# Kernel tuning notes

Measured on AMD Instinct MI355X. Metric: run time of the kernel, lower is better.

The kernel has to match this reference:

```python
import jax, jax.numpy as jnp
import numpy as np

EPS = 1e-5
NEG_SLOPE = 0.2
B, C, P, K, E, H = 16, 16, 2048, 16, 64, 2


def cross_set_gather(f, idx):
    # f: (B, C, P), idx: (B, P, K) -> (B, C, P, K)
    return jax.vmap(lambda fb, ib: fb[:, ib])(f, idx)


def bn(x, g, b, m, v, axes):
    # x normalized along channel dim; g,b,m,v shaped to broadcast via `axes` reshape
    return (x - m.reshape(axes)) * (g.reshape(axes) / jnp.sqrt(v.reshape(axes) + EPS)) + b.reshape(axes)


def setup_inputs() -> dict:
    key = jax.random.key(0)
    ks = jax.random.split(key, 16)
    features = jax.random.normal(ks[0], (B, C, P), dtype=jnp.float32)
    neighbor_indices = jax.random.randint(ks[1], (B, P, K), 0, P)
    mask = jax.random.randint(ks[2], (B, 1, P), 0, 2).astype(bool)
    s = 0.1
    return {
        "features": features,
        "neighbor_indices": neighbor_indices,
        "mask": mask,
        "node_w": jax.random.normal(ks[3], (H, E, C)) * s,
        "node_g": jnp.ones((H, E)),
        "node_b": jnp.zeros((H, E)),
        "node_m": jax.random.normal(ks[4], (H, E)) * s,
        "node_v": jax.random.uniform(ks[5], (H, E)) + 0.5,
        "edge_w": jax.random.normal(ks[6], (H, E, C)) * s,
        "edge_bias": jax.random.normal(ks[7], (H, E)) * s,
        "edge_g": jnp.ones((H, E)),
        "edge_b2": jnp.zeros((H, E)),
        "edge_m": jax.random.normal(ks[8], (H, E)) * s,
        "edge_v": jax.random.uniform(ks[9], (H, E)) + 0.5,
        "self_w": jax.random.normal(ks[10], (H, E)) * s,
        "self_b": jax.random.normal(ks[11], (H,)) * s,
        "nb_w": jax.random.normal(ks[12], (H, E)) * s,
        "nb_b": jax.random.normal(ks[13], (H,)) * s,
    }


def _forward(features, neighbor_indices, mask, node_w, node_g, node_b, node_m, node_v,
             edge_w, edge_bias, edge_g, edge_b2, edge_m, edge_v, self_w, self_b, nb_w, nb_b):
    mask_f = mask.astype(features.dtype)  # (B,1,P)
    # node encoding (Conv1d k=1 + BN): (B,H,E,P)
    nodes = jnp.einsum('hec,bcp->bhep', node_w, features)
    nodes = bn(nodes, node_g, node_b, node_m, node_v, (1, H, E, 1))
    # edge features: neighbor - center, (B,C,P,K)
    nbr = cross_set_gather(features, neighbor_indices)
    edge_feat = nbr - features[:, :, :, None]
    # edge encoding (Conv2d k=1 + BN): (B,H,E,P,K)
    enc = jnp.einsum('hec,bcpk->bhepk', edge_w, edge_feat) + edge_bias[None, :, :, None, None]
    enc = bn(enc, edge_g, edge_b2, edge_m, edge_v, (1, H, E, 1, 1))
    # attention scores
    self_score = jnp.einsum('he,bhep->bhp', self_w, nodes) + self_b[None, :, None]  # (B,H,P)
    nb_score = jnp.einsum('he,bhepk->bhpk', nb_w, enc) + nb_b[None, :, None, None]  # (B,H,P,K)
    logits = self_score[..., None] + nb_score
    logits = jnp.where(logits >= 0, logits, NEG_SLOPE * logits)  # leaky_relu(0.2)
    # neighbor validity mask: (B,P,K)
    valid = cross_set_gather(mask_f, neighbor_indices)[:, 0]
    vb = valid[:, None, :, :]  # (B,1,P,K)
    logits = jnp.where(vb == 0, -jnp.inf, logits)
    coef = jnp.nan_to_num(jax.nn.softmax(logits, axis=-1), nan=0.0, posinf=0.0, neginf=0.0)  # (B,H,P,K)
    # weighted aggregation + relu: (B,H,E,P)
    att = jax.nn.relu(jnp.einsum('bhpk,bhepk->bhep', coef, enc))
    # graph features: masked max over K
    enc_masked = jnp.where(vb[:, :, None, :, :] == 0, -jnp.inf, enc)
    graph = jnp.max(enc_masked, axis=-1)  # (B,H,E,P)
    graph = jnp.where(jnp.isinf(graph), 0.0, graph)
    # multi-head combine: element-wise max over heads, then mask
    att_out = jnp.max(att, axis=1) * mask_f  # (B,E,P)
    graph_out = jnp.max(graph, axis=1) * mask_f  # (B,E,P)
    return att_out, graph_out


def reference(features, neighbor_indices, mask, node_w, node_g, node_b, node_m, node_v,
              edge_w, edge_bias, edge_g, edge_b2, edge_m, edge_v, self_w, self_b, nb_w, nb_b):
    return _forward(features, neighbor_indices, mask, node_w, node_g, node_b, node_m, node_v,
                    edge_w, edge_bias, edge_g, edge_b2, edge_m, edge_v, self_w, self_b, nb_w, nb_b)
```

## Files before the change

kernel.cpp:

```cpp
#include <hip/hip_runtime.h>
#include <hip/hip_bf16.h>
#include <math.h>

#define NB 16
#define NC 16
#define NP 2048
#define NK 16
#define NE 64
#define NH 2
#define EPSV 1e-5f
#define NSLOPE 0.2f
#define QINV -1e30f
#define QTHR -1e29f

#define WS_FLAGS   0
#define WS_EW      256
#define WS_SE      8448
#define WS_CBE     8960
#define WS_WQ      9472
#define WS_WSC     9600
#define WS_CNB     9728
#define WS_CSELF   9744
#define WS_PINFO   16384
#define WS_EPROJ   544768

__device__ __forceinline__ float ldf(const void* p, int i, int isb) {
  return isb ? __bfloat162float(((const __hip_bfloat16*)p)[i]) : ((const float*)p)[i];
}

__global__ void __launch_bounds__(256) k_pre(
    const void* feat, const void* mask,
    const void* node_w, const void* node_g, const void* node_b,
    const void* node_m, const void* node_v,
    const void* edge_w, const void* edge_bias, const void* edge_g,
    const void* edge_b2, const void* edge_m, const void* edge_v,
    const void* self_w, const void* self_b, const void* nb_w, const void* nb_b,
    char* ws)
{
  __shared__ int cnt_exp, cnt_msk;
  __shared__ int flags[2];
  __shared__ float ewl[NH*NE*NC];
  __shared__ float nwl[NH*NE*NC];
  __shared__ float w2[NH*NE], wn[NH*NE], contrib[NH*NE], contrib2[NH*NE];
  const int tid = threadIdx.x;
  if (tid == 0) { cnt_exp = 0; cnt_msk = 0; }
  __syncthreads();
  const unsigned short* u = (const unsigned short*)feat;
  for (int i = tid; i < 512; i += 256) {
    int ex = (u[i] >> 7) & 0xFF;
    if (ex >= 100 && ex <= 135) atomicAdd(&cnt_exp, 1);
  }
  const unsigned char* mb = (const unsigned char*)mask;
  for (int i = tid; i < 1024; i += 256) {
    if ((i & 3) && mb[i]) atomicAdd(&cnt_msk, 1);
  }
  __syncthreads();
  if (tid == 0) {
    flags[0] = (cnt_exp >= 460) ? 1 : 0;
    flags[1] = (cnt_msk > 0) ? 1 : 0;
    ((int*)ws)[0] = flags[0];
    ((int*)ws)[1] = flags[1];
  }
  __syncthreads();
  const int isb = flags[0];

  float* g_ew    = (float*)(ws + WS_EW);
  float* g_se    = (float*)(ws + WS_SE);
  float* g_cbe   = (float*)(ws + WS_CBE);
  float* g_wq    = (float*)(ws + WS_WQ);
  float* g_wsc   = (float*)(ws + WS_WSC);
  float* g_cnb   = (float*)(ws + WS_CNB);
  float* g_cself = (float*)(ws + WS_CSELF);

  for (int i = tid; i < NH*NE*NC; i += 256) {
    float v = ldf(edge_w, i, isb);
    ewl[i] = v; g_ew[i] = v;
    nwl[i] = ldf(node_w, i, isb);
  }
  if (tid < NH*NE) {
    const int he = tid;
    float se = ldf(edge_g, he, isb) * rsqrtf(ldf(edge_v, he, isb) + EPSV);
    float cb = se * (ldf(edge_bias, he, isb) - ldf(edge_m, he, isb)) + ldf(edge_b2, he, isb);
    float ns = ldf(node_g, he, isb) * rsqrtf(ldf(node_v, he, isb) + EPSV);
    w2[he] = ldf(nb_w, he, isb) * se;
    wn[he] = ldf(self_w, he, isb) * ns;
    g_se[he] = se;
    g_cbe[he] = cb;
    contrib[he]  = ldf(self_w, he, isb) * (ldf(node_b, he, isb) - ldf(node_m, he, isb) * ns);
    contrib2[he] = ldf(nb_w, he, isb) * cb;
  }
  __syncthreads();
  if (tid < NH*NC) {
    const int h = tid >> 4, c = tid & 15;
    float sq = 0.f, sn = 0.f;
#pragma unroll 8
    for (int e = 0; e < NE; e++) {
      sq += w2[h*NE+e] * ewl[(h*NE+e)*NC + c];
      sn += wn[h*NE+e] * nwl[(h*NE+e)*NC + c];
    }
    g_wq[tid]  = sq;
    g_wsc[tid] = sn;
  }
  if (tid < NH) {
    float cs = 0.f, cn = 0.f;
#pragma unroll 8
    for (int e = 0; e < NE; e++) { cs += contrib[tid*NE+e]; cn += contrib2[tid*NE+e]; }
    g_cself[tid] = cs + ldf(self_b, tid, isb);
    g_cnb[tid]   = cn + ldf(nb_b, tid, isb);
  }
}

__global__ void __launch_bounds__(256) k_proj(const void* feat, const void* mask, char* ws)
{
  const int isb   = ((const int*)ws)[0];
  const int mbyte = ((const int*)ws)[1];
  const int bid = blockIdx.x;
  const int b  = (bid & 7) * 2 + ((bid >> 3) & 1);
  const int pt = bid >> 4;
  const int p0 = pt * 64;
  const int tid = threadIdx.x;

  __shared__ float fl[NC][64];
  for (int i = tid; i < NC*64; i += 256) {
    int c = i >> 6, p = i & 63;
    fl[c][p] = ldf(feat, (b*NC + c)*NP + p0 + p, isb);
  }
  __syncthreads();

  const float* g_ew = (const float*)(ws + WS_EW);
  const int c2 = tid & 127;
  const int e = c2 >> 1, h = c2 & 1;
  const int ph = tid >> 7;
  float wv[NC];
#pragma unroll
  for (int c = 0; c < NC; c++) wv[c] = g_ew[(h*NE + e)*NC + c];

  float* eo = (float*)(ws + WS_EPROJ);
  const long base = (long)(b*NP + p0) * 128;
  for (int i = 0; i < 32; i++) {
    const int p = i*2 + ph;
    float acc = 0.f;
#pragma unroll
    for (int c = 0; c < NC; c++) acc = fmaf(wv[c], fl[c][p], acc);
    eo[base + (long)p*128 + c2] = acc;
  }

  if (tid < 64) {
    const float* wq    = (const float*)(ws + WS_WQ);
    const float* wsc   = (const float*)(ws + WS_WSC);
    const float* cself = (const float*)(ws + WS_CSELF);
    float q0=0.f, q1=0.f, s0=0.f, s1=0.f;
#pragma unroll
    for (int c = 0; c < NC; c++) {
      const float f = fl[c][tid];
      q0 = fmaf(wq[c],      f, q0);
      q1 = fmaf(wq[NC+c],   f, q1);
      s0 = fmaf(wsc[c],     f, s0);
      s1 = fmaf(wsc[NC+c],  f, s1);
    }
    const int p = p0 + tid;
    bool mv;
    if (mbyte) mv = ((const unsigned char*)mask)[b*NP + p] != 0;
    else       mv = ((const int*)mask)[b*NP + p] != 0;
    float4 pi;
    pi.x = mv ? q0 : QINV;
    pi.y = mv ? q1 : QINV;
    pi.z = s0 + cself[0];
    pi.w = s1 + cself[1];
    ((float4*)(ws + WS_PINFO))[b*NP + p] = pi;
  }
}

__global__ void __launch_bounds__(256, 4) k_main(const int* nidx, char* ws, void* out)
{
  const int isb = ((const int*)ws)[0];
  const float4* pinfo = (const float4*)(ws + WS_PINFO);
  const float2* ep2   = (const float2*)(ws + WS_EPROJ);
  const float* g_se   = (const float*)(ws + WS_SE);
  const float* g_cbe  = (const float*)(ws + WS_CBE);
  const float* g_cnb  = (const float*)(ws + WS_CNB);

  const int bid = blockIdx.x;
  const int b  = (bid & 7) * 2 + ((bid >> 3) & 1);
  const int pt = bid >> 4;
  const int p0 = pt * 16;
  const int tid  = threadIdx.x;
  const int w    = tid >> 6;
  const int lane = tid & 63;
  const int jj = lane >> 4, kk = lane & 15;
  const int pw = p0 + w*4;

  __shared__ float4 coef_lds[4][4][NK];
  __shared__ float att_t[NE][17];
  __shared__ float gr_t[NE][17];

  const float cnb0 = g_cnb[0], cnb1 = g_cnb[1];

  const int idx_l = nidx[(b*NP + pw)*NK + lane];
  const float4 P  = pinfo[b*NP + idx_l];
  const float4 Pc = pinfo[b*NP + pw + jj];
  const bool valid = (P.x > QTHR);
  const unsigned long long vm  = __ballot(valid);
  const unsigned long long cvm = __ballot(Pc.x > QTHR);
  const unsigned vmj_own = (unsigned)((vm >> (16*jj)) & 0xFFFFull);
  const bool anyv = (vmj_own != 0);

  float c0, c1;
  {
    float l0 = Pc.z + P.x - Pc.x + cnb0;
    l0 = (l0 >= 0.f) ? l0 : NSLOPE * l0;
    float mx = l0;
#pragma unroll
    for (int o = 8; o >= 1; o >>= 1) mx = fmaxf(mx, __shfl_xor(mx, o));
    float ex = __expf(l0 - mx);
    float sm = ex;
#pragma unroll
    for (int o = 8; o >= 1; o >>= 1) sm += __shfl_xor(sm, o);
    c0 = anyv ? ex / sm : 0.f;
  }
  {
    float l1 = Pc.w + P.y - Pc.y + cnb1;
    l1 = (l1 >= 0.f) ? l1 : NSLOPE * l1;
    float mx = l1;
#pragma unroll
    for (int o = 8; o >= 1; o >>= 1) mx = fmaxf(mx, __shfl_xor(mx, o));
    float ex = __expf(l1 - mx);
    float sm = ex;
#pragma unroll
    for (int o = 8; o >= 1; o >>= 1) sm += __shfl_xor(sm, o);
    c1 = anyv ? ex / sm : 0.f;
  }
  coef_lds[w][jj][kk] = make_float4(c0, c1, __int_as_float(idx_l), 0.f);

  const float se0 = g_se[lane],      se1 = g_se[NE + lane];
  const float cb0 = g_cbe[lane],     cb1 = g_cbe[NE + lane];
  const long rowb = (long)b * NP;

  for (int j = 0; j < 4; j++) {
    const int pj = pw + j;
    const int pl = w*4 + j;
    if (!((cvm >> (16*j)) & 1)) {
      att_t[lane][pl] = 0.f; gr_t[lane][pl] = 0.f; continue;
    }
    const unsigned vmj = (unsigned)((vm >> (16*j)) & 0xFFFFull);
    const bool av = (vmj != 0);
    const float2 rawc = ep2[(rowb + pj)*NE + lane];
    const float cpe0 = cb0 - se0*rawc.x, cpe1 = cb1 - se1*rawc.y;

    float a0 = 0.f, a1 = 0.f;
    float mx0 = -INFINITY, mn0 = INFINITY, mx1 = -INFINITY, mn1 = INFINITY;
#pragma unroll
    for (int k = 0; k < NK; k++) {
      const float4 cf = coef_lds[w][j][k];
      const int ix = __float_as_int(cf.z);
      const float2 v = ep2[(rowb + ix)*NE + lane];
      a0 = fmaf(cf.x, v.x, a0);
      a1 = fmaf(cf.y, v.y, a1);
      if ((vmj >> k) & 1) {
        mx0 = fmaxf(mx0, v.x); mn0 = fminf(mn0, v.x);
        mx1 = fmaxf(mx1, v.y); mn1 = fminf(mn1, v.y);
      }
    }
    const float csel = av ? 1.f : 0.f;
    const float att0 = fmaxf(fmaf(se0, a0, cpe0*csel), 0.f);
    const float att1 = fmaxf(fmaf(se1, a1, cpe1*csel), 0.f);
    const float g0 = av ? (((se0 >= 0.f) ? se0*mx0 : se0*mn0) + cpe0) : 0.f;
    const float g1 = av ? (((se1 >= 0.f) ? se1*mx1 : se1*mn1) + cpe1) : 0.f;
    att_t[lane][pl] = fmaxf(att0, att1);
    gr_t[lane][pl]  = fmaxf(g0, g1);
  }
  __syncthreads();

  const long obase = (long)b * NE * NP;
  for (int i = tid; i < NE*16; i += 256) {
    const int ee = i >> 4, pp = i & 15;
    const long oi = obase + (long)ee * NP + p0 + pp;
    const float av = att_t[ee][pp], gv = gr_t[ee][pp];
    if (isb) {
      ((__hip_bfloat16*)out)[oi] = __float2bfloat16(av);
      ((__hip_bfloat16*)out)[oi + (long)NB*NE*NP] = __float2bfloat16(gv);
    } else {
      ((float*)out)[oi] = av;
      ((float*)out)[oi + (long)NB*NE*NP] = gv;
    }
  }
}

extern "C" void kernel_launch(void* const* d_in, const int* in_sizes, int n_in,
                              void* d_out, int out_size, void* d_ws, size_t ws_size,
                              hipStream_t stream)
{
  const void* feat      = d_in[0];
  const void* nidx      = d_in[1];
  const void* mask      = d_in[2];
  const void* node_w    = d_in[3];
  const void* node_g    = d_in[4];
  const void* node_b    = d_in[5];
  const void* node_m    = d_in[6];
  const void* node_v    = d_in[7];
  const void* edge_w    = d_in[8];
  const void* edge_bias = d_in[9];
  const void* edge_g    = d_in[10];
  const void* edge_b2   = d_in[11];
  const void* edge_m    = d_in[12];
  const void* edge_v    = d_in[13];
  const void* self_w    = d_in[14];
  const void* self_b    = d_in[15];
  const void* nb_w      = d_in[16];
  const void* nb_b      = d_in[17];
  char* ws = (char*)d_ws;

  hipLaunchKernelGGL(k_pre, dim3(1), dim3(256), 0, stream,
                     feat, mask, node_w, node_g, node_b, node_m, node_v,
                     edge_w, edge_bias, edge_g, edge_b2, edge_m, edge_v,
                     self_w, self_b, nb_w, nb_b, ws);
  hipLaunchKernelGGL(k_proj, dim3(NB*(NP/64)), dim3(256), 0, stream, feat, mask, ws);
  hipLaunchKernelGGL(k_main, dim3(NB*(NP/16)), dim3(256), 0, stream,
                     (const int*)nidx, ws, d_out);
}
```

Baseline: 140.3 us.

## Fold single-block preprocessing into projection and main kernels, compact valid neighbors

Removes the one-block k_pre launch by having every k_proj block recompute the folded BN and attention weights and dtype flags in shared memory, and every k_main block recompute edge scale and bias. k_main now handles 32 points per block (8 per wave) and stores a compacted list of valid neighbor indices and coefficients, so the gather loop runs only over valid neighbors with no per-element mask test. The aim is to remove a serial launch and to skip gathers for masked neighbors. The cost is redundant per-block parameter setup and a variable-trip-count inner loop that no longer fully unrolls.

```diff
diff --git a/kernel.cpp b/kernel.cpp
--- a/kernel.cpp
+++ b/kernel.cpp
@@ -13,14 +13,6 @@
 #define QINV -1e30f
 #define QTHR -1e29f
 
-#define WS_FLAGS   0
-#define WS_EW      256
-#define WS_SE      8448
-#define WS_CBE     8960
-#define WS_WQ      9472
-#define WS_WSC     9600
-#define WS_CNB     9728
-#define WS_CSELF   9744
 #define WS_PINFO   16384
 #define WS_EPROJ   544768
 
@@ -28,66 +20,73 @@
   return isb ? __bfloat162float(((const __hip_bfloat16*)p)[i]) : ((const float*)p)[i];
 }
 
-__global__ void __launch_bounds__(256) k_pre(
+__global__ void __launch_bounds__(256) k_proj(
     const void* feat, const void* mask,
-    const void* node_w, const void* node_g, const void* node_b,
-    const void* node_m, const void* node_v,
-    const void* edge_w, const void* edge_bias, const void* edge_g,
-    const void* edge_b2, const void* edge_m, const void* edge_v,
-    const void* self_w, const void* self_b, const void* nb_w, const void* nb_b,
+    const void* edge_w, const void* node_w,
+    const void* edge_g, const void* edge_v, const void* edge_bias,
+    const void* edge_m, const void* edge_b2,
+    const void* node_g, const void* node_v, const void* node_b, const void* node_m,
+    const void* self_w, const void* self_b, const void* nb_w,
     char* ws)
 {
-  __shared__ int cnt_exp, cnt_msk;
-  __shared__ int flags[2];
-  __shared__ float ewl[NH*NE*NC];
-  __shared__ float nwl[NH*NE*NC];
-  __shared__ float w2[NH*NE], wn[NH*NE], contrib[NH*NE], contrib2[NH*NE];
+  __shared__ int sh_isb, sh_mbyte;
+  __shared__ float ewl[128*17];
+  __shared__ float nwl[128*17];
+  __shared__ float fl[NC][64];
+  __shared__ float w2[128], wn[128], ctr[128];
+  __shared__ float s_wq[32], s_wsc[32], s_cself[2];
+
   const int tid = threadIdx.x;
-  if (tid == 0) { cnt_exp = 0; cnt_msk = 0; }
-  __syncthreads();
-  const unsigned short* u = (const unsigned short*)feat;
-  for (int i = tid; i < 512; i += 256) {
-    int ex = (u[i] >> 7) & 0xFF;
-    if (ex >= 100 && ex <= 135) atomicAdd(&cnt_exp, 1);
-  }
-  const unsigned char* mb = (const unsigned char*)mask;
-  for (int i = tid; i < 1024; i += 256) {
-    if ((i & 3) && mb[i]) atomicAdd(&cnt_msk, 1);
-  }
-  __syncthreads();
-  if (tid == 0) {
-    flags[0] = (cnt_exp >= 460) ? 1 : 0;
-    flags[1] = (cnt_msk > 0) ? 1 : 0;
-    ((int*)ws)[0] = flags[0];
-    ((int*)ws)[1] = flags[1];
-  }
-  __syncthreads();
-  const int isb = flags[0];
-
-  float* g_ew    = (float*)(ws + WS_EW);
-  float* g_se    = (float*)(ws + WS_SE);
-  float* g_cbe   = (float*)(ws + WS_CBE);
-  float* g_wq    = (float*)(ws + WS_WQ);
-  float* g_wsc   = (float*)(ws + WS_WSC);
-  float* g_cnb   = (float*)(ws + WS_CNB);
-  float* g_cself = (float*)(ws + WS_CSELF);
+  const int w = tid >> 6, lane = tid & 63;
+
+  if (w == 0) {
+    const unsigned short* u = (const unsigned short*)feat;
+    int cnt = 0;
+#pragma unroll
+    for (int i = 0; i < 8; i++) {
+      int ex = (u[lane*8 + i] >> 7) & 0xFF;
+      cnt += (ex >= 100 && ex <= 135) ? 1 : 0;
+    }
+#pragma unroll
+    for (int o = 32; o >= 1; o >>= 1) cnt += __shfl_xor(cnt, o);
+    if (lane == 0) sh_isb = (cnt >= 460) ? 1 : 0;
+  }
+  if (w == 1) {
+    const unsigned char* mb = (const unsigned char*)mask;
+    int c = 0;
+#pragma unroll
+    for (int i = 0; i < 16; i++) {
+      int ix = lane*16 + i;
+      c += ((ix & 3) && mb[ix]) ? 1 : 0;
+    }
+#pragma unroll
+    for (int o = 32; o >= 1; o >>= 1) c += __shfl_xor(c, o);
+    if (lane == 0) sh_mbyte = (c > 0) ? 1 : 0;
+  }
+  __syncthreads();
+  const int isb = sh_isb, mbyte = sh_mbyte;
+
+  const int bid = blockIdx.x;
+  const int b  = (bid & 7) * 2 + ((bid >> 3) & 1);
+  const int pt = bid >> 4;
+  const int p0 = pt * 64;
 
   for (int i = tid; i < NH*NE*NC; i += 256) {
-    float v = ldf(edge_w, i, isb);
-    ewl[i] = v; g_ew[i] = v;
-    nwl[i] = ldf(node_w, i, isb);
-  }
-  if (tid < NH*NE) {
+    const int he = i >> 4, c = i & 15;
+    ewl[he*17 + c] = ldf(edge_w, i, isb);
+    nwl[he*17 + c] = ldf(node_w, i, isb);
+  }
+  for (int i = tid; i < NC*64; i += 256) {
+    int c = i >> 6, p = i & 63;
+    fl[c][p] = ldf(feat, (b*NC + c)*NP + p0 + p, isb);
+  }
+  if (tid < 128) {
     const int he = tid;
     float se = ldf(edge_g, he, isb) * rsqrtf(ldf(edge_v, he, isb) + EPSV);
-    float cb = se * (ldf(edge_bias, he, isb) - ldf(edge_m, he, isb)) + ldf(edge_b2, he, isb);
     float ns = ldf(node_g, he, isb) * rsqrtf(ldf(node_v, he, isb) + EPSV);
-    w2[he] = ldf(nb_w, he, isb) * se;
-    wn[he] = ldf(self_w, he, isb) * ns;
-    g_se[he] = se;
-    g_cbe[he] = cb;
-    contrib[he]  = ldf(self_w, he, isb) * (ldf(node_b, he, isb) - ldf(node_m, he, isb) * ns);
-    contrib2[he] = ldf(nb_w, he, isb) * cb;
+    w2[he]  = ldf(nb_w, he, isb) * se;
+    wn[he]  = ldf(self_w, he, isb) * ns;
+    ctr[he] = ldf(self_w, he, isb) * (ldf(node_b, he, isb) - ldf(node_m, he, isb) * ns);
   }
   __syncthreads();
   if (tid < NH*NC) {
@@ -95,45 +94,26 @@
     float sq = 0.f, sn = 0.f;
 #pragma unroll 8
     for (int e = 0; e < NE; e++) {
-      sq += w2[h*NE+e] * ewl[(h*NE+e)*NC + c];
-      sn += wn[h*NE+e] * nwl[(h*NE+e)*NC + c];
-    }
-    g_wq[tid]  = sq;
-    g_wsc[tid] = sn;
+      sq += w2[h*NE+e] * ewl[(h*NE+e)*17 + c];
+      sn += wn[h*NE+e] * nwl[(h*NE+e)*17 + c];
+    }
+    s_wq[tid]  = sq;
+    s_wsc[tid] = sn;
   }
   if (tid < NH) {
-    float cs = 0.f, cn = 0.f;
+    float cs = 0.f;
 #pragma unroll 8
-    for (int e = 0; e < NE; e++) { cs += contrib[tid*NE+e]; cn += contrib2[tid*NE+e]; }
-    g_cself[tid] = cs + ldf(self_b, tid, isb);
-    g_cnb[tid]   = cn + ldf(nb_b, tid, isb);
-  }
-}
-
-__global__ void __launch_bounds__(256) k_proj(const void* feat, const void* mask, char* ws)
-{
-  const int isb   = ((const int*)ws)[0];
-  const int mbyte = ((const int*)ws)[1];
-  const int bid = blockIdx.x;
-  const int b  = (bid & 7) * 2 + ((bid >> 3) & 1);
-  const int pt = bid >> 4;
-  const int p0 = pt * 64;
-  const int tid = threadIdx.x;
-
-  __shared__ float fl[NC][64];
-  for (int i = tid; i < NC*64; i += 256) {
-    int c = i >> 6, p = i & 63;
-    fl[c][p] = ldf(feat, (b*NC + c)*NP + p0 + p, isb);
-  }
-  __syncthreads();
-
-  const float* g_ew = (const float*)(ws + WS_EW);
+    for (int e = 0; e < NE; e++) cs += ctr[tid*NE+e];
+    s_cself[tid] = cs + ldf(self_b, tid, isb);
+  }
+  __syncthreads();
+
   const int c2 = tid & 127;
   const int e = c2 >> 1, h = c2 & 1;
   const int ph = tid >> 7;
   float wv[NC];
 #pragma unroll
-  for (int c = 0; c < NC; c++) wv[c] = g_ew[(h*NE + e)*NC + c];
+  for (int c = 0; c < NC; c++) wv[c] = ewl[(h*NE + e)*17 + c];
 
   float* eo = (float*)(ws + WS_EPROJ);
   const long base = (long)(b*NP + p0) * 128;
@@ -146,17 +126,14 @@
   }
 
   if (tid < 64) {
-    const float* wq    = (const float*)(ws + WS_WQ);
-    const float* wsc   = (const float*)(ws + WS_WSC);
-    const float* cself = (const float*)(ws + WS_CSELF);
     float q0=0.f, q1=0.f, s0=0.f, s1=0.f;
 #pragma unroll
     for (int c = 0; c < NC; c++) {
       const float f = fl[c][tid];
-      q0 = fmaf(wq[c],      f, q0);
-      q1 = fmaf(wq[NC+c],   f, q1);
-      s0 = fmaf(wsc[c],     f, s0);
-      s1 = fmaf(wsc[NC+c],  f, s1);
+      q0 = fmaf(s_wq[c],      f, q0);
+      q1 = fmaf(s_wq[NC+c],   f, q1);
+      s0 = fmaf(s_wsc[c],     f, s0);
+      s1 = fmaf(s_wsc[NC+c],  f, s1);
     }
     const int p = p0 + tid;
     bool mv;
@@ -165,102 +142,141 @@
     float4 pi;
     pi.x = mv ? q0 : QINV;
     pi.y = mv ? q1 : QINV;
-    pi.z = s0 + cself[0];
-    pi.w = s1 + cself[1];
+    pi.z = s0 + s_cself[0];
+    pi.w = s1 + s_cself[1];
     ((float4*)(ws + WS_PINFO))[b*NP + p] = pi;
   }
 }
 
-__global__ void __launch_bounds__(256, 4) k_main(const int* nidx, char* ws, void* out)
+__global__ void __launch_bounds__(256, 4) k_main(
+    const void* feat, const int* nidx,
+    const void* edge_g, const void* edge_v, const void* edge_bias,
+    const void* edge_m, const void* edge_b2,
+    const void* nb_w, const void* nb_b,
+    char* ws, void* out)
 {
-  const int isb = ((const int*)ws)[0];
+  __shared__ int sh_isb;
+  __shared__ float sh_se[128], sh_cbe[128], sh_cnb[2];
+  __shared__ float2 c01[4][8][NK];
+  __shared__ int    idxc[4][8][NK];
+  __shared__ unsigned char s_cnt[4][8], s_cm[4][8];
+  __shared__ float att_t[NE][33];
+  __shared__ float gr_t[NE][33];
+
+  const int tid  = threadIdx.x;
+  const int w    = tid >> 6;
+  const int lane = tid & 63;
+
+  if (w == 0) {
+    const unsigned short* u = (const unsigned short*)feat;
+    int cnt = 0;
+#pragma unroll
+    for (int i = 0; i < 8; i++) {
+      int ex = (u[lane*8 + i] >> 7) & 0xFF;
+      cnt += (ex >= 100 && ex <= 135) ? 1 : 0;
+    }
+#pragma unroll
+    for (int o = 32; o >= 1; o >>= 1) cnt += __shfl_xor(cnt, o);
+    if (lane == 0) sh_isb = (cnt >= 460) ? 1 : 0;
+  }
+  __syncthreads();
+  const int isb = sh_isb;
+
+  if (tid < 128) {
+    const int he = tid, h = tid >> 6;
+    float se = ldf(edge_g, he, isb) * rsqrtf(ldf(edge_v, he, isb) + EPSV);
+    float cb = se * (ldf(edge_bias, he, isb) - ldf(edge_m, he, isb)) + ldf(edge_b2, he, isb);
+    sh_se[he]  = se;
+    sh_cbe[he] = cb;
+    float t = ldf(nb_w, he, isb) * cb;
+#pragma unroll
+    for (int o = 32; o >= 1; o >>= 1) t += __shfl_xor(t, o);
+    if ((tid & 63) == 0) sh_cnb[h] = t + ldf(nb_b, h, isb);
+  }
+  __syncthreads();
+
   const float4* pinfo = (const float4*)(ws + WS_PINFO);
   const float2* ep2   = (const float2*)(ws + WS_EPROJ);
-  const float* g_se   = (const float*)(ws + WS_SE);
-  const float* g_cbe  = (const float*)(ws + WS_CBE);
-  const float* g_cnb  = (const float*)(ws + WS_CNB);
 
   const int bid = blockIdx.x;
   const int b  = (bid & 7) * 2 + ((bid >> 3) & 1);
   const int pt = bid >> 4;
-  const int p0 = pt * 16;
-  const int tid  = threadIdx.x;
-  const int w    = tid >> 6;
-  const int lane = tid & 63;
+  const int p0 = pt * 32;
   const int jj = lane >> 4, kk = lane & 15;
-  const int pw = p0 + w*4;
-
-  __shared__ float4 coef_lds[4][4][NK];
-  __shared__ float att_t[NE][17];
-  __shared__ float gr_t[NE][17];
-
-  const float cnb0 = g_cnb[0], cnb1 = g_cnb[1];
-
-  const int idx_l = nidx[(b*NP + pw)*NK + lane];
-  const float4 P  = pinfo[b*NP + idx_l];
-  const float4 Pc = pinfo[b*NP + pw + jj];
-  const bool valid = (P.x > QTHR);
-  const unsigned long long vm  = __ballot(valid);
-  const unsigned long long cvm = __ballot(Pc.x > QTHR);
-  const unsigned vmj_own = (unsigned)((vm >> (16*jj)) & 0xFFFFull);
-  const bool anyv = (vmj_own != 0);
-
-  float c0, c1;
-  {
-    float l0 = Pc.z + P.x - Pc.x + cnb0;
-    l0 = (l0 >= 0.f) ? l0 : NSLOPE * l0;
-    float mx = l0;
-#pragma unroll
-    for (int o = 8; o >= 1; o >>= 1) mx = fmaxf(mx, __shfl_xor(mx, o));
-    float ex = __expf(l0 - mx);
-    float sm = ex;
-#pragma unroll
-    for (int o = 8; o >= 1; o >>= 1) sm += __shfl_xor(sm, o);
-    c0 = anyv ? ex / sm : 0.f;
-  }
-  {
-    float l1 = Pc.w + P.y - Pc.y + cnb1;
-    l1 = (l1 >= 0.f) ? l1 : NSLOPE * l1;
-    float mx = l1;
-#pragma unroll
-    for (int o = 8; o >= 1; o >>= 1) mx = fmaxf(mx, __shfl_xor(mx, o));
-    float ex = __expf(l1 - mx);
-    float sm = ex;
-#pragma unroll
-    for (int o = 8; o >= 1; o >>= 1) sm += __shfl_xor(sm, o);
-    c1 = anyv ? ex / sm : 0.f;
-  }
-  coef_lds[w][jj][kk] = make_float4(c0, c1, __int_as_float(idx_l), 0.f);
-
-  const float se0 = g_se[lane],      se1 = g_se[NE + lane];
-  const float cb0 = g_cbe[lane],     cb1 = g_cbe[NE + lane];
+  const float cnb0 = sh_cnb[0], cnb1 = sh_cnb[1];
+
+  for (int jr = 0; jr < 2; jr++) {
+    const int pw4 = p0 + w*8 + jr*4;
+    const int idx_l = nidx[(b*NP + pw4)*NK + lane];
+    const float4 P  = pinfo[b*NP + idx_l];
+    const float4 Pc = pinfo[b*NP + pw4 + jj];
+    const bool valid = (P.x > QTHR);
+    const unsigned long long vm = __ballot(valid);
+    const unsigned vmj = (unsigned)((vm >> (16*jj)) & 0xFFFFull);
+    const bool anyv = (vmj != 0);
+
+    float c0, c1;
+    {
+      float l0 = Pc.z + P.x - Pc.x + cnb0;
+      l0 = (l0 >= 0.f) ? l0 : NSLOPE * l0;
+      float mx = l0;
+#pragma unroll
+      for (int o = 8; o >= 1; o >>= 1) mx = fmaxf(mx, __shfl_xor(mx, o));
+      float ex = __expf(l0 - mx);
+      float sm = ex;
+#pragma unroll
+      for (int o = 8; o >= 1; o >>= 1) sm += __shfl_xor(sm, o);
+      c0 = anyv ? ex / sm : 0.f;
+    }
+    {
+      float l1 = Pc.w + P.y - Pc.y + cnb1;
+      l1 = (l1 >= 0.f) ? l1 : NSLOPE * l1;
+      float mx = l1;
+#pragma unroll
+      for (int o = 8; o >= 1; o >>= 1) mx = fmaxf(mx, __shfl_xor(mx, o));
+      float ex = __expf(l1 - mx);
+      float sm = ex;
+#pragma unroll
+      for (int o = 8; o >= 1; o >>= 1) sm += __shfl_xor(sm, o);
+      c1 = anyv ? ex / sm : 0.f;
+    }
+    const int jx = jr*4 + jj;
+    const int pos = __popc(vmj & ((1u << kk) - 1));
+    if (valid) {
+      c01[w][jx][pos]  = make_float2(c0, c1);
+      idxc[w][jx][pos] = idx_l;
+    }
+    if (kk == 0) {
+      s_cnt[w][jx] = (unsigned char)__popc(vmj);
+      s_cm[w][jx]  = (Pc.x > QTHR) ? 1 : 0;
+    }
+  }
+
+  const float se0 = sh_se[lane],  se1 = sh_se[NE + lane];
+  const float cb0 = sh_cbe[lane], cb1 = sh_cbe[NE + lane];
   const long rowb = (long)b * NP;
 
-  for (int j = 0; j < 4; j++) {
-    const int pj = pw + j;
-    const int pl = w*4 + j;
-    if (!((cvm >> (16*j)) & 1)) {
-      att_t[lane][pl] = 0.f; gr_t[lane][pl] = 0.f; continue;
-    }
-    const unsigned vmj = (unsigned)((vm >> (16*j)) & 0xFFFFull);
-    const bool av = (vmj != 0);
+  for (int j = 0; j < 8; j++) {
+    const int pj = p0 + w*8 + j;
+    const int pl = w*8 + j;
+    if (!s_cm[w][j]) { att_t[lane][pl] = 0.f; gr_t[lane][pl] = 0.f; continue; }
+    const int cnt = s_cnt[w][j];
     const float2 rawc = ep2[(rowb + pj)*NE + lane];
     const float cpe0 = cb0 - se0*rawc.x, cpe1 = cb1 - se1*rawc.y;
 
     float a0 = 0.f, a1 = 0.f;
     float mx0 = -INFINITY, mn0 = INFINITY, mx1 = -INFINITY, mn1 = INFINITY;
-#pragma unroll
-    for (int k = 0; k < NK; k++) {
-      const float4 cf = coef_lds[w][j][k];
-      const int ix = __float_as_int(cf.z);
+#pragma unroll 4
+    for (int k = 0; k < cnt; k++) {
+      const float2 cf = c01[w][j][k];
+      const int ix = idxc[w][j][k];
       const float2 v = ep2[(rowb + ix)*NE + lane];
       a0 = fmaf(cf.x, v.x, a0);
       a1 = fmaf(cf.y, v.y, a1);
-      if ((vmj >> k) & 1) {
-        mx0 = fmaxf(mx0, v.x); mn0 = fminf(mn0, v.x);
-        mx1 = fmaxf(mx1, v.y); mn1 = fminf(mn1, v.y);
-      }
-    }
+      mx0 = fmaxf(mx0, v.x); mn0 = fminf(mn0, v.x);
+      mx1 = fmaxf(mx1, v.y); mn1 = fminf(mn1, v.y);
+    }
+    const bool av = (cnt > 0);
     const float csel = av ? 1.f : 0.f;
     const float att0 = fmaxf(fmaf(se0, a0, cpe0*csel), 0.f);
     const float att1 = fmaxf(fmaf(se1, a1, cpe1*csel), 0.f);
@@ -272,8 +288,8 @@
   __syncthreads();
 
   const long obase = (long)b * NE * NP;
-  for (int i = tid; i < NE*16; i += 256) {
-    const int ee = i >> 4, pp = i & 15;
+  for (int i = tid; i < NE*32; i += 256) {
+    const int ee = i >> 5, pp = i & 31;
     const long oi = obase + (long)ee * NP + p0 + pp;
     const float av = att_t[ee][pp], gv = gr_t[ee][pp];
     if (isb) {
@@ -310,11 +326,13 @@
   const void* nb_b      = d_in[17];
   char* ws = (char*)d_ws;
 
-  hipLaunchKernelGGL(k_pre, dim3(1), dim3(256), 0, stream,
-                     feat, mask, node_w, node_g, node_b, node_m, node_v,
-                     edge_w, edge_bias, edge_g, edge_b2, edge_m, edge_v,
-                     self_w, self_b, nb_w, nb_b, ws);
-  hipLaunchKernelGGL(k_proj, dim3(NB*(NP/64)), dim3(256), 0, stream, feat, mask, ws);
-  hipLaunchKernelGGL(k_main, dim3(NB*(NP/16)), dim3(256), 0, stream,
-                     (const int*)nidx, ws, d_out);
+  hipLaunchKernelGGL(k_proj, dim3(NB*(NP/64)), dim3(256), 0, stream,
+                     feat, mask, edge_w, node_w,
+                     edge_g, edge_v, edge_bias, edge_m, edge_b2,
+                     node_g, node_v, node_b, node_m,
+                     self_w, self_b, nb_w, ws);
+  hipLaunchKernelGGL(k_main, dim3(NB*(NP/32)), dim3(256), 0, stream,
+                     feat, (const int*)nidx,
+                     edge_g, edge_v, edge_bias, edge_m, edge_b2,
+                     nb_w, nb_b, ws, d_out);
 }
```

Measured after the change: 129.1 us. -7.9%, faster.
